# Performance work log

Measured on AMD Instinct MI355X. Metric: run time of the kernel, lower is better.

Reference implementation:

```python
import jax, jax.numpy as jnp
import numpy as np
from jax import lax

BETA, THETA = 0.9, 1.0

# snntorch atan surrogate (alpha=2): fwd Heaviside, bwd 1/(1+(pi*u)^2)
@jax.custom_vjp
def spike(u):
    return (u > 0).astype(u.dtype)

def _spike_fwd(u):
    return (u > 0).astype(u.dtype), u

def _spike_bwd(u, g):
    return (g / (1.0 + (jnp.pi * u) ** 2),)

spike.defvjp(_spike_fwd, _spike_bwd)

def lif(cur, mem):
    # snntorch Leaky, reset_mechanism='subtract': reset from PREVIOUS mem (detached)
    reset = lax.stop_gradient((mem > THETA).astype(mem.dtype))
    mem = BETA * mem + cur - reset * THETA
    spk = spike(mem - THETA)
    return spk, mem

def conv1d(x, w, b, stride, pad):
    y = lax.conv_general_dilated(x, w, (stride,), [(pad, pad)],
                                 dimension_numbers=('NCW', 'OIW', 'NCW'))
    return y + b[None, :, None]

def maxpool2(x):
    return lax.reduce_window(x, -jnp.inf, lax.max, (1, 1, 2), (1, 1, 2), 'VALID')

def setup_inputs():
    key = jax.random.key(0)
    ks = jax.random.split(key, 9)
    B, T, L = 512, 100, 686
    def u(k, shape, fan_in):
        lim = 1.0 / np.sqrt(fan_in)
        return jax.random.uniform(k, shape, jnp.float32, -lim, lim)
    return {
        'x': jax.random.normal(ks[0], (B, T, 1, L), jnp.float32),
        'w1': u(ks[1], (16, 1, 13), 13), 'b1': u(ks[2], (16,), 13),
        'w2': u(ks[3], (32, 16, 7), 16 * 7), 'b2': u(ks[4], (32,), 16 * 7),
        'wf1': u(ks[5], (32, 32 * 22), 32 * 22), 'bf1': u(ks[6], (32,), 32 * 22),
        'wf2': u(ks[7], (2, 32), 32), 'bf2': u(ks[8], (2,), 32),
    }

def reference(x, w1, b1, w2, b2, wf1, bf1, wf2, bf2):
    B, T, C, L = x.shape
    mem0 = (jnp.zeros((B, 16, 136), x.dtype),  # after conv1
            jnp.zeros((B, 32, 22), x.dtype),   # after conv2
            jnp.zeros((B, 32), x.dtype),       # after fc1
            jnp.zeros((B, 2), x.dtype))        # after fc2
    xT = jnp.transpose(x, (1, 0, 2, 3))  # [T, B, 1, L]

    def step(carry, xt):
        mem1, mem2, mem3, mem4 = carry
        h = conv1d(xt, w1, b1, 5, 1)          # [B,16,136]
        spk1, mem1 = lif(h, mem1)
        h = maxpool2(spk1)                    # [B,16,68]
        h = conv1d(h, w2, b2, 3, 1)           # [B,32,22]
        spk2, mem2 = lif(h, mem2)
        h = spk2.reshape(B, -1)               # [B,704]
        h = h @ wf1.T + bf1                   # [B,32]
        spk3, mem3 = lif(h, mem3)
        h = spk3 @ wf2.T + bf2                # [B,2]
        spk4, mem4 = lif(h, mem4)
        return (mem1, mem2, mem3, mem4), spk4

    _, spks = lax.scan(step, mem0, xT)
    # inference path (train=False): sum of output spikes over timesteps
    return spks.sum(axis=0)
```

## Files before the change

### kernel.cpp

```cpp
#include <hip/hip_runtime.h>
#include <stdint.h>


#define NB 512
#define NT 100
#define LIN 686
#define RS 71

typedef float v2f __attribute__((ext_vector_type(2)));

__device__ __forceinline__ v2f pkfma(v2f a, v2f b, v2f c) {
    v2f d;
    asm("v_pk_fma_f32 %0, %1, %2, %3" : "=v"(d) : "v"(a), "v"(b), "v"(c));
    return d;
}

__device__ __forceinline__ float dpp_add8(float x) {
    int t;
    t = __builtin_amdgcn_mov_dpp(__float_as_int(x), 0x141, 0xf, 0xf, true);
    x += __int_as_float(t);
    t = __builtin_amdgcn_mov_dpp(__float_as_int(x), 0x1B, 0xf, 0xf, true);
    x += __int_as_float(t);
    t = __builtin_amdgcn_mov_dpp(__float_as_int(x), 0xB1, 0xf, 0xf, true);
    x += __int_as_float(t);
    return x;
}

__device__ __forceinline__ float red32(float x) {
    int t;
    t = __builtin_amdgcn_mov_dpp(__float_as_int(x), 0xB1, 0xf, 0xf, true);
    x += __int_as_float(t);
    t = __builtin_amdgcn_mov_dpp(__float_as_int(x), 0x4E, 0xf, 0xf, true);
    x += __int_as_float(t);
    t = __builtin_amdgcn_ds_swizzle(__float_as_int(x), 0x101F);
    x += __int_as_float(t);
    t = __builtin_amdgcn_ds_swizzle(__float_as_int(x), 0x201F);
    x += __int_as_float(t);
    t = __builtin_amdgcn_ds_swizzle(__float_as_int(x), 0x401F);
    x += __int_as_float(t);
    return x;
}

__global__
__attribute__((amdgpu_flat_work_group_size(512, 512)))
__attribute__((amdgpu_waves_per_eu(1, 2)))
void snn_all(
    const float* __restrict__ x,
    const float* __restrict__ w1, const float* __restrict__ b1,
    const float* __restrict__ w2, const float* __restrict__ b2,
    const float* __restrict__ wf1, const float* __restrict__ bf1,
    const float* __restrict__ wf2, const float* __restrict__ bf2,
    float* __restrict__ out)
{
    __shared__ __align__(16) float swf1r[5632 * 4];
    __shared__ __align__(16) float sx[2][LIN + 2];
    __shared__ __align__(16) float spool2f[2][8 * RS * 2];
    __shared__ unsigned long long sbits[2][4][3];
    __shared__ __align__(16) float sspk3[2][32];

    const int tid  = threadIdx.x;
    const int h    = tid >> 8;
    const int t2   = tid & 255;
    const int b    = blockIdx.x * 2 + h;
    const int lane = t2 & 63;
    const int wv   = t2 >> 6;

    float* sxh    = sx[h];
    float* spoolh = spool2f[h];
    unsigned long long (*sbh)[3] = sbits[h];
    float* sspk3h = sspk3[h];

    for (int d = tid; d < 5632; d += 512) {
        int wvd = d / 1408;
        int r   = d - wvd * 1408;
        int i   = r >> 6;
        int l   = r & 63;
        int gg  = (l >> 5) & 1;
        int s   = l & 31;
        int jb0 = wvd * 8 + gg * 4;
        int ii  = (i < 11) ? i : (i - 11);
        int j0  = (i < 11) ? jb0 : (jb0 + 2);
        float4 v;
        v.x = wf1[(j0 + 0) * 704 + s * 22 + 2 * ii];
        v.y = wf1[(j0 + 0) * 704 + s * 22 + 2 * ii + 1];
        v.z = wf1[(j0 + 1) * 704 + s * 22 + 2 * ii];
        v.w = wf1[(j0 + 1) * 704 + s * 22 + 2 * ii + 1];
        reinterpret_cast<float4*>(swf1r)[d] = v;
    }

    const int ca = t2 & 15;
    const int pg = t2 >> 4;
    float wA[13];
    #pragma unroll
    for (int k = 0; k < 13; ++k) wA[k] = w1[ca * 13 + k];
    v2f we0 = {wA[0], wA[1]}, we1 = {wA[2], wA[3]}, we2 = {wA[4], wA[5]},
        we3 = {wA[6], wA[7]}, we4 = {wA[8], wA[9]}, we5 = {wA[10], wA[11]};
    v2f wo0 = {wA[1], wA[2]}, wo1 = {wA[3], wA[4]}, wo2 = {wA[5], wA[6]},
        wo3 = {wA[7], wA[8]}, wo4 = {wA[9], wA[10]}, wo5 = {wA[11], wA[12]};
    const float wA0s = wA[0], wA12s = wA[12];
    const float bA = b1[ca];
    float m1a[5], m1b[5];
    #pragma unroll
    for (int j = 0; j < 5; ++j) { m1a[j] = 0.f; m1b[j] = 0.f; }

    const int ip = lane & 7;
    const int X  = lane >> 3;
    const int og = X & 3;
    const int cg = X >> 2;
    const int ccq = ip & 3;
    const int chO = wv * 8 + cg * 4 + ccq;
    v2f wp0[7], wp1[7], wp2[7], wp3[7];
    #pragma unroll
    for (int k = 0; k < 7; ++k) {
        int base0 = (wv * 8 + cg * 4 + 0) * 112 + 14 * ip + k;
        int base1 = (wv * 8 + cg * 4 + 1) * 112 + 14 * ip + k;
        int base2 = (wv * 8 + cg * 4 + 2) * 112 + 14 * ip + k;
        int base3 = (wv * 8 + cg * 4 + 3) * 112 + 14 * ip + k;
        wp0[k].x = w2[base0]; wp0[k].y = w2[base0 + 7];
        wp1[k].x = w2[base1]; wp1[k].y = w2[base1 + 7];
        wp2[k].x = w2[base2]; wp2[k].y = w2[base2 + 7];
        wp3[k].x = w2[base3]; wp3[k].y = w2[base3 + 7];
    }
    const float bB = b2[chO];
    float m2r0 = 0.f, m2r1 = 0.f, m2r2 = 0.f;

    const int gg = (t2 >> 5) & 1;
    const int s_ = t2 & 31;
    const int jb = wv * 8 + gg * 4;
    float bC0 = bf1[jb], bC1 = bf1[jb + 1], bC2 = bf1[jb + 2], bC3 = bf1[jb + 3];
    float m30 = 0.f, m31 = 0.f, m32 = 0.f, m33 = 0.f;
    const int cbsh = ((s_ >> 2) & 1) * 32 + (s_ & 3);

    float wD = 0.f, bD = 0.f;
    if (t2 < 64) {
        wD = wf2[(t2 >> 5) * 32 + (t2 & 31)];
        if ((t2 & 31) == 0) bD = bf2[t2 >> 5];
    }
    float m4 = 0.f, cnt = 0.f;

    for (int i = t2; i < 8 * RS * 2; i += 256) spoolh[i] = 0.f;
    const float* xb = x + (size_t)b * NT * LIN;
    if (t2 == 0) { sxh[0] = 0.f; sxh[LIN + 1] = 0.f; }
    sxh[1 + t2]       = xb[t2];
    sxh[1 + t2 + 256] = xb[t2 + 256];
    if (t2 < LIN - 512) sxh[1 + t2 + 512] = xb[t2 + 512];
    __syncthreads();

    const v2f* spool2v = reinterpret_cast<const v2f*>(spoolh);
    const v2f* wb = spool2v + ip * RS + 3 * og;
    const float4* swfv = reinterpret_cast<const float4*>(swf1r);
    const float4* wrow = swfv + (wv * 22) * 64 + lane;

#define A_J(j) { \
    const int p_ = ((j) == 4) ? (64 + pg) : (pg + 16 * (j)); \
    if ((j) < 4 || pg < 4) { \
        const v2f* qv_ = reinterpret_cast<const v2f*>(sxh + 10 * p_); \
        v2f q0_ = qv_[0], q1_ = qv_[1], q2_ = qv_[2], q3_ = qv_[3], q4_ = qv_[4], \
            q5_ = qv_[5], q6_ = qv_[6], q7_ = qv_[7], q8_ = qv_[8]; \
        v2f va_ = {0.f, 0.f}, vb_ = {0.f, 0.f}; \
        va_ = pkfma(we0, q0_, va_); va_ = pkfma(we1, q1_, va_); \
        va_ = pkfma(we2, q2_, va_); va_ = pkfma(we3, q3_, va_); \
        va_ = pkfma(we4, q4_, va_); va_ = pkfma(we5, q5_, va_); \
        vb_ = pkfma(wo0, q3_, vb_); vb_ = pkfma(wo1, q4_, vb_); \
        vb_ = pkfma(wo2, q5_, vb_); vb_ = pkfma(wo3, q6_, vb_); \
        vb_ = pkfma(wo4, q7_, vb_); vb_ = pkfma(wo5, q8_, vb_); \
        float a0_ = (va_.x + va_.y) + wA12s * q6_.x; \
        float a1_ = (vb_.x + vb_.y) + wA0s * q2_.y; \
        float m0_ = m1a[(j)], mm_ = m1b[(j)]; \
        float r0_ = (m0_ > 1.f) ? 1.f : 0.f; \
        float r1_ = (mm_ > 1.f) ? 1.f : 0.f; \
        m0_ = 0.9f * m0_ + (a0_ + bA) - r0_; \
        mm_ = 0.9f * mm_ + (a1_ + bA) - r1_; \
        m1a[(j)] = m0_; m1b[(j)] = mm_; \
        spoolh[((ca >> 1) * RS + 1 + p_) * 2 + (ca & 1)] = \
            (m0_ > 1.f || mm_ > 1.f) ? 1.f : 0.f; \
    } }

#define B_WIN(om, MSLOT, SPK) { \
    v2f t0_ = wb[(om) * 12 + 0], t1_ = wb[(om) * 12 + 1], t2v_ = wb[(om) * 12 + 2], \
        t3_ = wb[(om) * 12 + 3], t4_ = wb[(om) * 12 + 4], t5_ = wb[(om) * 12 + 5], \
        t6_ = wb[(om) * 12 + 6]; \
    v2f a0_ = {0.f, 0.f}, a1_ = {0.f, 0.f}, a2_ = {0.f, 0.f}, a3_ = {0.f, 0.f}; \
    a0_ = pkfma(wp0[0], t0_, a0_); a1_ = pkfma(wp1[0], t0_, a1_); \
    a2_ = pkfma(wp2[0], t0_, a2_); a3_ = pkfma(wp3[0], t0_, a3_); \
    a0_ = pkfma(wp0[1], t1_, a0_); a1_ = pkfma(wp1[1], t1_, a1_); \
    a2_ = pkfma(wp2[1], t1_, a2_); a3_ = pkfma(wp3[1], t1_, a3_); \
    a0_ = pkfma(wp0[2], t2v_, a0_); a1_ = pkfma(wp1[2], t2v_, a1_); \
    a2_ = pkfma(wp2[2], t2v_, a2_); a3_ = pkfma(wp3[2], t2v_, a3_); \
    a0_ = pkfma(wp0[3], t3_, a0_); a1_ = pkfma(wp1[3], t3_, a1_); \
    a2_ = pkfma(wp2[3], t3_, a2_); a3_ = pkfma(wp3[3], t3_, a3_); \
    a0_ = pkfma(wp0[4], t4_, a0_); a1_ = pkfma(wp1[4], t4_, a1_); \
    a2_ = pkfma(wp2[4], t4_, a2_); a3_ = pkfma(wp3[4], t4_, a3_); \
    a0_ = pkfma(wp0[5], t5_, a0_); a1_ = pkfma(wp1[5], t5_, a1_); \
    a2_ = pkfma(wp2[5], t5_, a2_); a3_ = pkfma(wp3[5], t5_, a3_); \
    a0_ = pkfma(wp0[6], t6_, a0_); a1_ = pkfma(wp1[6], t6_, a1_); \
    a2_ = pkfma(wp2[6], t6_, a2_); a3_ = pkfma(wp3[6], t6_, a3_); \
    float s0_ = dpp_add8(a0_.x + a0_.y); \
    float s1_ = dpp_add8(a1_.x + a1_.y); \
    float s2_ = dpp_add8(a2_.x + a2_.y); \
    float s3_ = dpp_add8(a3_.x + a3_.y); \
    float sc_ = (ccq == 0) ? s0_ : ((ccq == 1) ? s1_ : ((ccq == 2) ? s2_ : s3_)); \
    if ((ip >> 2) == ((om) & 1)) { \
        float mm_ = MSLOT; \
        float rr_ = (mm_ > 1.f) ? 1.f : 0.f; \
        mm_ = 0.9f * mm_ + (sc_ + bB) - rr_; \
        MSLOT = mm_; \
        SPK = (mm_ > 1.f) ? 1.f : 0.f; \
    } }

    for (int t = 0; t < NT; ++t) {
        A_J(0) A_J(1) A_J(2) A_J(3) A_J(4)
        __syncthreads();

        float xp0 = 0.f, xp1 = 0.f, xp2 = 0.f;
        if (t + 1 < NT) {
            const float* xt = xb + (size_t)(t + 1) * LIN;
            xp0 = xt[t2];
            xp1 = xt[t2 + 256];
            if (t2 < LIN - 512) xp2 = xt[t2 + 512];
        }

        float spk0 = 0.f, spk1 = 0.f, spk2 = 0.f;
        B_WIN(0, m2r0, spk0)
        B_WIN(1, m2r0, spk0)
        B_WIN(2, m2r1, spk1)
        B_WIN(3, m2r1, spk1)
        B_WIN(4, m2r2, spk2)
        if (og < 2) { B_WIN(5, m2r2, spk2) }

        {
            unsigned long long bal0 = __ballot(spk0 > 0.5f);
            unsigned long long bal1 = __ballot(spk1 > 0.5f);
            unsigned long long bal2 = __ballot(spk2 > 0.5f);
            if (lane == 0) {
                sbh[wv][0] = bal0;
                sbh[wv][1] = bal1;
                sbh[wv][2] = bal2;
            }
        }

        if (t + 1 < NT) {
            sxh[1 + t2]       = xp0;
            sxh[1 + t2 + 256] = xp1;
            if (t2 < LIN - 512) sxh[1 + t2 + 512] = xp2;
        }
        __syncthreads();

        {
            unsigned long long M0 = sbh[s_ >> 3][0];
            unsigned long long M1 = sbh[s_ >> 3][1];
            unsigned long long M2 = sbh[s_ >> 3][2];
            uint32_t W0 = (uint32_t)(M0 >> cbsh);
            uint32_t W1 = (uint32_t)(M1 >> cbsh);
            uint32_t W2 = (uint32_t)(M2 >> cbsh);

            v2f a0v = {0.f, 0.f}, a1v = {0.f, 0.f}, a2v = {0.f, 0.f}, a3v = {0.f, 0.f};
            #pragma unroll
            for (int i = 0; i < 11; ++i) {
                const int o0 = 2 * i, o1 = 2 * i + 1;
                uint32_t wl0 = (o0 < 8) ? W0 : ((o0 < 16) ? W1 : W2);
                uint32_t wl1 = (o1 < 8) ? W0 : ((o1 < 16) ? W1 : W2);
                v2f fpi;
                fpi.x = (float)((wl0 >> ((o0 & 3) * 8 + ((o0 >> 2) & 1) * 4)) & 1u);
                fpi.y = (float)((wl1 >> ((o1 & 3) * 8 + ((o1 >> 2) & 1) * 4)) & 1u);
                float4 wa  = wrow[i * 64];
                float4 wb4 = wrow[(11 + i) * 64];
                a0v = pkfma((v2f){wa.x,  wa.y},  fpi, a0v);
                a1v = pkfma((v2f){wa.z,  wa.w},  fpi, a1v);
                a2v = pkfma((v2f){wb4.x, wb4.y}, fpi, a2v);
                a3v = pkfma((v2f){wb4.z, wb4.w}, fpi, a3v);
            }
            float a0 = red32(a0v.x + a0v.y);
            float a1 = red32(a1v.x + a1v.y);
            float a2 = red32(a2v.x + a2v.y);
            float a3 = red32(a3v.x + a3v.y);

            float r0 = (m30 > 1.f) ? 1.f : 0.f; m30 = 0.9f * m30 + (a0 + bC0) - r0;
            float r1 = (m31 > 1.f) ? 1.f : 0.f; m31 = 0.9f * m31 + (a1 + bC1) - r1;
            float r2 = (m32 > 1.f) ? 1.f : 0.f; m32 = 0.9f * m32 + (a2 + bC2) - r2;
            float r3 = (m33 > 1.f) ? 1.f : 0.f; m33 = 0.9f * m33 + (a3 + bC3) - r3;
            if (s_ == 0) {
                float4 st;
                st.x = (m30 > 1.f) ? 1.f : 0.f;
                st.y = (m31 > 1.f) ? 1.f : 0.f;
                st.z = (m32 > 1.f) ? 1.f : 0.f;
                st.w = (m33 > 1.f) ? 1.f : 0.f;
                *reinterpret_cast<float4*>(&sspk3h[jb]) = st;
            }
        }
        __syncthreads();

        if (t2 < 64) {
            float v = sspk3h[t2 & 31] * wD;
            v += __shfl_xor(v, 16, 32);
            v += __shfl_xor(v, 8, 32);
            v += __shfl_xor(v, 4, 32);
            v += __shfl_xor(v, 2, 32);
            v += __shfl_xor(v, 1, 32);
            if ((t2 & 31) == 0) {
                float rr = (m4 > 1.f) ? 1.f : 0.f;
                m4 = 0.9f * m4 + (v + bD) - rr;
                if (m4 > 1.f) cnt += 1.f;
            }
        }
    }

    if (t2 == 0)  out[b * 2 + 0] = cnt;
    if (t2 == 32) out[b * 2 + 1] = cnt;
}

extern "C" void kernel_launch(void* const* d_in, const int* in_sizes, int n_in,
                              void* d_out, int out_size, void* d_ws, size_t ws_size,
                              hipStream_t stream) {
    const float* x   = (const float*)d_in[0];
    const float* w1  = (const float*)d_in[1];
    const float* b1  = (const float*)d_in[2];
    const float* w2  = (const float*)d_in[3];
    const float* b2  = (const float*)d_in[4];
    const float* wf1 = (const float*)d_in[5];
    const float* bf1 = (const float*)d_in[6];
    const float* wf2 = (const float*)d_in[7];
    const float* bf2 = (const float*)d_in[8];
    float* out = (float*)d_out;

    snn_all<<<NB / 2, 512, 0, stream>>>(x, w1, b1, w2, b2, wf1, bf1, wf2, bf2, out);
}
```

Measured before the change: 404.7 us.

## Double threads per sample to 512 and repartition conv/fc work per wave

Launches 1024-thread blocks (512 threads per sample) instead of 512, halving per-thread work in every stage: conv1 positions, conv2 output windows and channels per wave, and fc1 outputs per thread. The fc1 weight layout in shared memory and the spike bitmask layout are reorganised to match the new mapping. The aim is to shorten the serial per-timestep critical path of the recurrent scan by spreading it over more waves. The cost is more threads taking part in the block-wide barriers, fewer registers per thread, and reduction overhead that is duplicated across more lanes.

```diff
diff --git a/kernel.cpp b/kernel.cpp
--- a/kernel.cpp
+++ b/kernel.cpp
@@ -42,8 +42,7 @@
 }
 
 __global__
-__attribute__((amdgpu_flat_work_group_size(512, 512)))
-__attribute__((amdgpu_waves_per_eu(1, 2)))
+__attribute__((amdgpu_flat_work_group_size(1024, 1024)))
 void snn_all(
     const float* __restrict__ x,
     const float* __restrict__ w1, const float* __restrict__ b1,
@@ -55,36 +54,31 @@
     __shared__ __align__(16) float swf1r[5632 * 4];
     __shared__ __align__(16) float sx[2][LIN + 2];
     __shared__ __align__(16) float spool2f[2][8 * RS * 2];
-    __shared__ unsigned long long sbits[2][4][3];
-    __shared__ __align__(16) float sspk3[2][32];
+    __shared__ unsigned long long sbits2[2][8][2];
+    __shared__ __align__(8) float sspk3[2][32];
 
     const int tid  = threadIdx.x;
-    const int h    = tid >> 8;
-    const int t2   = tid & 255;
+    const int h    = tid >> 9;
+    const int t2   = tid & 511;
     const int b    = blockIdx.x * 2 + h;
     const int lane = t2 & 63;
     const int wv   = t2 >> 6;
 
     float* sxh    = sx[h];
     float* spoolh = spool2f[h];
-    unsigned long long (*sbh)[3] = sbits[h];
+    unsigned long long (*sbh)[2] = sbits2[h];
     float* sspk3h = sspk3[h];
 
-    for (int d = tid; d < 5632; d += 512) {
-        int wvd = d / 1408;
-        int r   = d - wvd * 1408;
-        int i   = r >> 6;
-        int l   = r & 63;
-        int gg  = (l >> 5) & 1;
-        int s   = l & 31;
-        int jb0 = wvd * 8 + gg * 4;
-        int ii  = (i < 11) ? i : (i - 11);
-        int j0  = (i < 11) ? jb0 : (jb0 + 2);
+    for (int d = tid; d < 5632; d += 1024) {
+        int g = d / 352;
+        int r = d - g * 352;
+        int i = r >> 5;
+        int s = r & 31;
         float4 v;
-        v.x = wf1[(j0 + 0) * 704 + s * 22 + 2 * ii];
-        v.y = wf1[(j0 + 0) * 704 + s * 22 + 2 * ii + 1];
-        v.z = wf1[(j0 + 1) * 704 + s * 22 + 2 * ii];
-        v.w = wf1[(j0 + 1) * 704 + s * 22 + 2 * ii + 1];
+        v.x = wf1[(2 * g)     * 704 + s * 22 + 2 * i];
+        v.y = wf1[(2 * g)     * 704 + s * 22 + 2 * i + 1];
+        v.z = wf1[(2 * g + 1) * 704 + s * 22 + 2 * i];
+        v.w = wf1[(2 * g + 1) * 704 + s * 22 + 2 * i + 1];
         reinterpret_cast<float4*>(swf1r)[d] = v;
     }
 
@@ -99,37 +93,36 @@
         wo3 = {wA[7], wA[8]}, wo4 = {wA[9], wA[10]}, wo5 = {wA[11], wA[12]};
     const float wA0s = wA[0], wA12s = wA[12];
     const float bA = b1[ca];
-    float m1a[5], m1b[5];
+    float m1a[3], m1b[3];
     #pragma unroll
-    for (int j = 0; j < 5; ++j) { m1a[j] = 0.f; m1b[j] = 0.f; }
-
-    const int ip = lane & 7;
-    const int X  = lane >> 3;
-    const int og = X & 3;
-    const int cg = X >> 2;
+    for (int j = 0; j < 3; ++j) { m1a[j] = 0.f; m1b[j] = 0.f; }
+
+    const int ip  = lane & 7;
+    const int og  = (lane >> 3) & 3;
+    const int omh = lane >> 5;
     const int ccq = ip & 3;
-    const int chO = wv * 8 + cg * 4 + ccq;
     v2f wp0[7], wp1[7], wp2[7], wp3[7];
     #pragma unroll
     for (int k = 0; k < 7; ++k) {
-        int base0 = (wv * 8 + cg * 4 + 0) * 112 + 14 * ip + k;
-        int base1 = (wv * 8 + cg * 4 + 1) * 112 + 14 * ip + k;
-        int base2 = (wv * 8 + cg * 4 + 2) * 112 + 14 * ip + k;
-        int base3 = (wv * 8 + cg * 4 + 3) * 112 + 14 * ip + k;
+        int base0 = (wv * 4 + 0) * 112 + 14 * ip + k;
+        int base1 = (wv * 4 + 1) * 112 + 14 * ip + k;
+        int base2 = (wv * 4 + 2) * 112 + 14 * ip + k;
+        int base3 = (wv * 4 + 3) * 112 + 14 * ip + k;
         wp0[k].x = w2[base0]; wp0[k].y = w2[base0 + 7];
         wp1[k].x = w2[base1]; wp1[k].y = w2[base1 + 7];
         wp2[k].x = w2[base2]; wp2[k].y = w2[base2 + 7];
         wp3[k].x = w2[base3]; wp3[k].y = w2[base3 + 7];
     }
-    const float bB = b2[chO];
-    float m2r0 = 0.f, m2r1 = 0.f, m2r2 = 0.f;
-
-    const int gg = (t2 >> 5) & 1;
-    const int s_ = t2 & 31;
-    const int jb = wv * 8 + gg * 4;
-    float bC0 = bf1[jb], bC1 = bf1[jb + 1], bC2 = bf1[jb + 2], bC3 = bf1[jb + 3];
-    float m30 = 0.f, m31 = 0.f, m32 = 0.f, m33 = 0.f;
-    const int cbsh = ((s_ >> 2) & 1) * 32 + (s_ & 3);
+    const float bB = b2[wv * 4 + ccq];
+    float mA = 0.f, mB = 0.f;
+
+    const int sub = (t2 >> 5) & 1;
+    const int gC  = wv * 2 + sub;
+    const int s_  = t2 & 31;
+    const float bC0 = bf1[2 * gC], bC1 = bf1[2 * gC + 1];
+    float m30 = 0.f, m31 = 0.f;
+    const int q_  = s_ >> 2;
+    const int cc_ = s_ & 3;
 
     float wD = 0.f, bD = 0.f;
     if (t2 < 64) {
@@ -138,22 +131,22 @@
     }
     float m4 = 0.f, cnt = 0.f;
 
-    for (int i = t2; i < 8 * RS * 2; i += 256) spoolh[i] = 0.f;
+    for (int i = t2; i < 8 * RS * 2; i += 512) spoolh[i] = 0.f;
     const float* xb = x + (size_t)b * NT * LIN;
     if (t2 == 0) { sxh[0] = 0.f; sxh[LIN + 1] = 0.f; }
-    sxh[1 + t2]       = xb[t2];
-    sxh[1 + t2 + 256] = xb[t2 + 256];
+    sxh[1 + t2] = xb[t2];
     if (t2 < LIN - 512) sxh[1 + t2 + 512] = xb[t2 + 512];
     __syncthreads();
 
     const v2f* spool2v = reinterpret_cast<const v2f*>(spoolh);
-    const v2f* wb = spool2v + ip * RS + 3 * og;
-    const float4* swfv = reinterpret_cast<const float4*>(swf1r);
-    const float4* wrow = swfv + (wv * 22) * 64 + lane;
+    const v2f* wb0 = spool2v + ip * RS + 3 * og + 12 * omh;
+    const v2f* wb1 = wb0 + 24;
+    const v2f* wb2 = wb0 + 48;
+    const float4* wrow = reinterpret_cast<const float4*>(swf1r) + gC * 352 + s_;
 
 #define A_J(j) { \
-    const int p_ = ((j) == 4) ? (64 + pg) : (pg + 16 * (j)); \
-    if ((j) < 4 || pg < 4) { \
+    const int p_ = ((j) == 2) ? (64 + pg) : (pg + 32 * (j)); \
+    if ((j) < 2 || pg < 4) { \
         const v2f* qv_ = reinterpret_cast<const v2f*>(sxh + 10 * p_); \
         v2f q0_ = qv_[0], q1_ = qv_[1], q2_ = qv_[2], q3_ = qv_[3], q4_ = qv_[4], \
             q5_ = qv_[5], q6_ = qv_[6], q7_ = qv_[7], q8_ = qv_[8]; \
@@ -176,10 +169,9 @@
             (m0_ > 1.f || mm_ > 1.f) ? 1.f : 0.f; \
     } }
 
-#define B_WIN(om, MSLOT, SPK) { \
-    v2f t0_ = wb[(om) * 12 + 0], t1_ = wb[(om) * 12 + 1], t2v_ = wb[(om) * 12 + 2], \
-        t3_ = wb[(om) * 12 + 3], t4_ = wb[(om) * 12 + 4], t5_ = wb[(om) * 12 + 5], \
-        t6_ = wb[(om) * 12 + 6]; \
+#define B_WIN(WB, COND, MSLOT, SPK) { \
+    v2f t0_ = (WB)[0], t1_ = (WB)[1], t2v_ = (WB)[2], t3_ = (WB)[3], \
+        t4_ = (WB)[4], t5_ = (WB)[5], t6_ = (WB)[6]; \
     v2f a0_ = {0.f, 0.f}, a1_ = {0.f, 0.f}, a2_ = {0.f, 0.f}, a3_ = {0.f, 0.f}; \
     a0_ = pkfma(wp0[0], t0_, a0_); a1_ = pkfma(wp1[0], t0_, a1_); \
     a2_ = pkfma(wp2[0], t0_, a2_); a3_ = pkfma(wp3[0], t0_, a3_); \
@@ -200,7 +192,7 @@
     float s2_ = dpp_add8(a2_.x + a2_.y); \
     float s3_ = dpp_add8(a3_.x + a3_.y); \
     float sc_ = (ccq == 0) ? s0_ : ((ccq == 1) ? s1_ : ((ccq == 2) ? s2_ : s3_)); \
-    if ((ip >> 2) == ((om) & 1)) { \
+    if (COND) { \
         float mm_ = MSLOT; \
         float rr_ = (mm_ > 1.f) ? 1.f : 0.f; \
         mm_ = 0.9f * mm_ + (sc_ + bB) - rr_; \
@@ -209,83 +201,68 @@
     } }
 
     for (int t = 0; t < NT; ++t) {
-        A_J(0) A_J(1) A_J(2) A_J(3) A_J(4)
+        A_J(0) A_J(1) A_J(2)
         __syncthreads();
 
-        float xp0 = 0.f, xp1 = 0.f, xp2 = 0.f;
+        float xp0 = 0.f, xp1 = 0.f;
         if (t + 1 < NT) {
             const float* xt = xb + (size_t)(t + 1) * LIN;
             xp0 = xt[t2];
-            xp1 = xt[t2 + 256];
-            if (t2 < LIN - 512) xp2 = xt[t2 + 512];
-        }
-
-        float spk0 = 0.f, spk1 = 0.f, spk2 = 0.f;
-        B_WIN(0, m2r0, spk0)
-        B_WIN(1, m2r0, spk0)
-        B_WIN(2, m2r1, spk1)
-        B_WIN(3, m2r1, spk1)
-        B_WIN(4, m2r2, spk2)
-        if (og < 2) { B_WIN(5, m2r2, spk2) }
+            if (t2 < LIN - 512) xp1 = xt[t2 + 512];
+        }
+
+        float spkA = 0.f, spkB = 0.f;
+        B_WIN(wb0, ip < 4,  mA, spkA)
+        B_WIN(wb1, ip >= 4, mA, spkA)
+        if (omh == 0 || og < 2) {
+            B_WIN(wb2, ip < 4, mB, spkB)
+        }
 
         {
-            unsigned long long bal0 = __ballot(spk0 > 0.5f);
-            unsigned long long bal1 = __ballot(spk1 > 0.5f);
-            unsigned long long bal2 = __ballot(spk2 > 0.5f);
-            if (lane == 0) {
-                sbh[wv][0] = bal0;
-                sbh[wv][1] = bal1;
-                sbh[wv][2] = bal2;
+            unsigned long long bal1 = __ballot(spkA > 0.5f);
+            unsigned long long bal2 = __ballot(spkB > 0.5f);
+            if (lane == 0) { sbh[wv][0] = bal1; sbh[wv][1] = bal2; }
+        }
+
+        if (t + 1 < NT) {
+            sxh[1 + t2] = xp0;
+            if (t2 < LIN - 512) sxh[1 + t2 + 512] = xp1;
+        }
+        __syncthreads();
+
+        {
+            unsigned long long Ms1 = sbh[q_][0] >> cc_;
+            unsigned long long Ms2 = sbh[q_][1] >> cc_;
+            uint32_t W1lo = (uint32_t)Ms1, W1hi = (uint32_t)(Ms1 >> 32);
+            uint32_t W2lo = (uint32_t)Ms2, W2hi = (uint32_t)(Ms2 >> 32);
+
+            float f[22];
+            #pragma unroll
+            for (int o = 0; o < 22; ++o) {
+                uint32_t w = (o < 16) ? (((o >> 2) & 1) ? W1hi : W1lo)
+                                      : (((o >> 2) & 1) ? W2hi : W2lo);
+                int sh = (o < 16) ? (4 * ((o >> 3) & 1) + 8 * (o & 3)) : (8 * (o & 3));
+                f[o] = (float)((w >> sh) & 1u);
             }
-        }
-
-        if (t + 1 < NT) {
-            sxh[1 + t2]       = xp0;
-            sxh[1 + t2 + 256] = xp1;
-            if (t2 < LIN - 512) sxh[1 + t2 + 512] = xp2;
-        }
-        __syncthreads();
-
-        {
-            unsigned long long M0 = sbh[s_ >> 3][0];
-            unsigned long long M1 = sbh[s_ >> 3][1];
-            unsigned long long M2 = sbh[s_ >> 3][2];
-            uint32_t W0 = (uint32_t)(M0 >> cbsh);
-            uint32_t W1 = (uint32_t)(M1 >> cbsh);
-            uint32_t W2 = (uint32_t)(M2 >> cbsh);
-
-            v2f a0v = {0.f, 0.f}, a1v = {0.f, 0.f}, a2v = {0.f, 0.f}, a3v = {0.f, 0.f};
+
+            v2f a0v = {0.f, 0.f}, a1v = {0.f, 0.f};
             #pragma unroll
             for (int i = 0; i < 11; ++i) {
-                const int o0 = 2 * i, o1 = 2 * i + 1;
-                uint32_t wl0 = (o0 < 8) ? W0 : ((o0 < 16) ? W1 : W2);
-                uint32_t wl1 = (o1 < 8) ? W0 : ((o1 < 16) ? W1 : W2);
-                v2f fpi;
-                fpi.x = (float)((wl0 >> ((o0 & 3) * 8 + ((o0 >> 2) & 1) * 4)) & 1u);
-                fpi.y = (float)((wl1 >> ((o1 & 3) * 8 + ((o1 >> 2) & 1) * 4)) & 1u);
-                float4 wa  = wrow[i * 64];
-                float4 wb4 = wrow[(11 + i) * 64];
-                a0v = pkfma((v2f){wa.x,  wa.y},  fpi, a0v);
-                a1v = pkfma((v2f){wa.z,  wa.w},  fpi, a1v);
-                a2v = pkfma((v2f){wb4.x, wb4.y}, fpi, a2v);
-                a3v = pkfma((v2f){wb4.z, wb4.w}, fpi, a3v);
+                v2f fpi = (v2f){f[2 * i], f[2 * i + 1]};
+                float4 wa = wrow[i * 32];
+                a0v = pkfma((v2f){wa.x, wa.y}, fpi, a0v);
+                a1v = pkfma((v2f){wa.z, wa.w}, fpi, a1v);
             }
             float a0 = red32(a0v.x + a0v.y);
             float a1 = red32(a1v.x + a1v.y);
-            float a2 = red32(a2v.x + a2v.y);
-            float a3 = red32(a3v.x + a3v.y);
 
             float r0 = (m30 > 1.f) ? 1.f : 0.f; m30 = 0.9f * m30 + (a0 + bC0) - r0;
             float r1 = (m31 > 1.f) ? 1.f : 0.f; m31 = 0.9f * m31 + (a1 + bC1) - r1;
-            float r2 = (m32 > 1.f) ? 1.f : 0.f; m32 = 0.9f * m32 + (a2 + bC2) - r2;
-            float r3 = (m33 > 1.f) ? 1.f : 0.f; m33 = 0.9f * m33 + (a3 + bC3) - r3;
             if (s_ == 0) {
-                float4 st;
+                float2 st;
                 st.x = (m30 > 1.f) ? 1.f : 0.f;
                 st.y = (m31 > 1.f) ? 1.f : 0.f;
-                st.z = (m32 > 1.f) ? 1.f : 0.f;
-                st.w = (m33 > 1.f) ? 1.f : 0.f;
-                *reinterpret_cast<float4*>(&sspk3h[jb]) = st;
+                *reinterpret_cast<float2*>(&sspk3h[2 * gC]) = st;
             }
         }
         __syncthreads();
@@ -323,5 +300,5 @@
     const float* bf2 = (const float*)d_in[8];
     float* out = (float*)d_out;
 
-    snn_all<<<NB / 2, 512, 0, stream>>>(x, w1, b1, w2, b2, wf1, bf1, wf2, bf2, out);
-}
+    snn_all<<<NB / 2, 1024, 0, stream>>>(x, w1, b1, w2, b2, wf1, bf1, wf2, bf2, out);
+}
```

Result: slower. 893.2 us (+120.7%).

## Software-pipeline timestep phases to drop one barrier per step

Applied to the files above, without the earlier changes.

Restructures the per-timestep schedule. The conv1 phase for step t+1 now runs after the mid-step barrier, alongside the fc1 phase of step t. The fc2 phase for step t-1 moves ahead of the ballot and barrier of step t, with a prologue and epilogue added to handle the first and last steps. This cuts three block-wide barriers per timestep to two and lets independent phases overlap, which shortens the serial chain across the 100 steps. In exchange the loop becomes harder to follow and may raise register pressure.

```diff
diff --git a/kernel.cpp b/kernel.cpp
--- a/kernel.cpp
+++ b/kernel.cpp
@@ -208,10 +208,25 @@
         SPK = (mm_ > 1.f) ? 1.f : 0.f; \
     } }
 
+#define PHASE_D() { \
+    if (t2 < 64) { \
+        float v = sspk3h[t2 & 31] * wD; \
+        v += __shfl_xor(v, 16, 32); \
+        v += __shfl_xor(v, 8, 32); \
+        v += __shfl_xor(v, 4, 32); \
+        v += __shfl_xor(v, 2, 32); \
+        v += __shfl_xor(v, 1, 32); \
+        if ((t2 & 31) == 0) { \
+            float rr = (m4 > 1.f) ? 1.f : 0.f; \
+            m4 = 0.9f * m4 + (v + bD) - rr; \
+            if (m4 > 1.f) cnt += 1.f; \
+        } \
+    } }
+
+    A_J(0) A_J(1) A_J(2) A_J(3) A_J(4)
+    __syncthreads();
+
     for (int t = 0; t < NT; ++t) {
-        A_J(0) A_J(1) A_J(2) A_J(3) A_J(4)
-        __syncthreads();
-
         float xp0 = 0.f, xp1 = 0.f, xp2 = 0.f;
         if (t + 1 < NT) {
             const float* xt = xb + (size_t)(t + 1) * LIN;
@@ -227,6 +242,8 @@
         B_WIN(3, m2r1, spk1)
         B_WIN(4, m2r2, spk2)
         if (og < 2) { B_WIN(5, m2r2, spk2) }
+
+        if (t > 0) { PHASE_D() }
 
         {
             unsigned long long bal0 = __ballot(spk0 > 0.5f);
@@ -245,6 +262,10 @@
             if (t2 < LIN - 512) sxh[1 + t2 + 512] = xp2;
         }
         __syncthreads();
+
+        if (t + 1 < NT) {
+            A_J(0) A_J(1) A_J(2) A_J(3) A_J(4)
+        }
 
         {
             unsigned long long M0 = sbh[s_ >> 3][0];
@@ -289,21 +310,9 @@
             }
         }
         __syncthreads();
-
-        if (t2 < 64) {
-            float v = sspk3h[t2 & 31] * wD;
-            v += __shfl_xor(v, 16, 32);
-            v += __shfl_xor(v, 8, 32);
-            v += __shfl_xor(v, 4, 32);
-            v += __shfl_xor(v, 2, 32);
-            v += __shfl_xor(v, 1, 32);
-            if ((t2 & 31) == 0) {
-                float rr = (m4 > 1.f) ? 1.f : 0.f;
-                m4 = 0.9f * m4 + (v + bD) - rr;
-                if (m4 > 1.f) cnt += 1.f;
-            }
-        }
     }
+
+    PHASE_D()
 
     if (t2 == 0)  out[b * 2 + 0] = cnt;
     if (t2 == 32) out[b * 2 + 1] = cnt;
```

Result: no change. 404.9 us (+0.0%).
